# Kernel tuning notes

Hardware: AMD Instinct MI355X
Metric: run time of the kernel (lower is better)

Reference implementation:

```python
import jax, jax.numpy as jnp
import numpy as np

N = 5000          # ngenes / nodes
IN_DIM = 1280
H = 128           # hid_dim
E = 160000        # edges (before self-loops)
ALPHA = 0.2       # LeakyReLU slope (both module leakyrelu and GATv2 negative_slope)

def _glorot(key, shape):
    fan_in, fan_out = shape[0], shape[-1]
    lim = jnp.sqrt(6.0 / (fan_in + fan_out))
    return jax.random.uniform(key, shape, jnp.float32, -lim, lim)

def setup_inputs() -> dict:
    key = jax.random.key(0)
    ks = jax.random.split(key, 12)
    x = jax.random.normal(ks[0], (N, IN_DIM), jnp.float32)
    edge_index = jax.random.randint(ks[1], (2, E), 0, N, jnp.int64)
    return {
        "x": x,
        "edge_index": edge_index,
        "W_in": _glorot(ks[2], (IN_DIM, H)),
        "b_in": jnp.zeros((H,), jnp.float32),
        "W_l": _glorot(ks[3], (H, H)),
        "b_l": jnp.zeros((H,), jnp.float32),
        "W_r": _glorot(ks[4], (H, H)),
        "b_r": jnp.zeros((H,), jnp.float32),
        "att": _glorot(ks[5], (H, 1))[:, 0],
        "gat_bias": jnp.zeros((H,), jnp.float32),
        "W1": _glorot(ks[6], (N * H, H)),
        "b1": jnp.zeros((H,), jnp.float32),
        "W2": _glorot(ks[7], (H, 1)),
        "b2": jnp.zeros((1,), jnp.float32),
    }

def _leaky(v):
    return jnp.where(v >= 0, v, ALPHA * v)

def _gatv2(x, edge_index, W_l, b_l, W_r, b_r, att, gat_bias):
    # add self loops (PyG default)
    loop = jnp.arange(N, dtype=edge_index.dtype)
    src = jnp.concatenate([edge_index[0], loop])  # j: source of message
    dst = jnp.concatenate([edge_index[1], loop])  # i: target / softmax segment
    xl = x @ W_l + b_l                             # [N, H] (messages)
    xr = x @ W_r + b_r                             # [N, H] (target side)
    e = _leaky(xl[src] + xr[dst])                  # [E+N, H]
    score = e @ att                                # [E+N]
    # segment softmax over incoming edges of each dst node
    m = jax.ops.segment_max(score, dst, num_segments=N)
    ex = jnp.exp(score - m[dst])
    s = jax.ops.segment_sum(ex, dst, num_segments=N)
    a = ex / s[dst]                                # [E+N]
    out = jax.ops.segment_sum(a[:, None] * xl[src], dst, num_segments=N)
    return out + gat_bias

def reference(x, edge_index, W_in, b_in, W_l, b_l, W_r, b_r, att, gat_bias, W1, b1, W2, b2):
    h = jax.nn.relu(x @ W_in + b_in)                               # [N, H]
    h = _leaky(_gatv2(h, edge_index, W_l, b_l, W_r, b_r, att, gat_bias))
    h = h.reshape(-1)                                              # [N*H]
    h = jax.nn.relu(h @ W1 + b1)                                   # [H]
    return h @ W2 + b2                                             # [1]
```

## Files before the change

kernel.cpp:

```cpp
#include <hip/hip_runtime.h>
#include <math.h>

#define N_NODES 5000
#define IN_DIM  1280
#define HID     128
#define ALPHA   0.2f

typedef float f4v __attribute__((ext_vector_type(4)));

__device__ __forceinline__ float leaky(float v) { return v >= 0.f ? v : ALPHA * v; }

__global__ __launch_bounds__(256) void k_gemm_in(const float* __restrict__ x,
    const float* __restrict__ W, float* __restrict__ hp) {
  const int col  = threadIdx.x & 127;
  const int rg   = threadIdx.x >> 7;
  const int row0 = blockIdx.x * 8;
  const int kbase = blockIdx.y * 640;
  __shared__ float xs[8][128];
  float acc[4] = {0.f,0.f,0.f,0.f};
  for (int k0 = 0; k0 < 640; k0 += 128) {
#pragma unroll
    for (int t = 0; t < 4; ++t) {
      int idx = threadIdx.x + t * 256;
      int r = idx >> 7, cc = idx & 127;
      xs[r][cc] = x[(size_t)(row0 + r) * IN_DIM + kbase + k0 + cc];
    }
    __syncthreads();
#pragma unroll 8
    for (int kq = 0; kq < 32; ++kq) {
      const int kk = kbase + k0 + kq * 4;
      const float w0 = W[(kk + 0) * HID + col];
      const float w1 = W[(kk + 1) * HID + col];
      const float w2 = W[(kk + 2) * HID + col];
      const float w3 = W[(kk + 3) * HID + col];
#pragma unroll
      for (int r = 0; r < 4; ++r) {
        const f4v xv = *reinterpret_cast<const f4v*>(&xs[rg * 4 + r][kq * 4]);
        acc[r] = fmaf(xv.x, w0, acc[r]);
        acc[r] = fmaf(xv.y, w1, acc[r]);
        acc[r] = fmaf(xv.z, w2, acc[r]);
        acc[r] = fmaf(xv.w, w3, acc[r]);
      }
    }
    __syncthreads();
  }
  float* o = hp + (size_t)blockIdx.y * N_NODES * HID;
#pragma unroll
  for (int r = 0; r < 4; ++r)
    o[(size_t)(row0 + rg * 4 + r) * HID + col] = acc[r];
}

__global__ __launch_bounds__(256) void k_gemm_lr(const float* __restrict__ hp,
    const float* __restrict__ bin,
    const float* __restrict__ Wl, const float* __restrict__ bl,
    const float* __restrict__ Wr, const float* __restrict__ br,
    float* __restrict__ xl, float* __restrict__ xr) {
  const int col  = threadIdx.x & 127;
  const int rg   = threadIdx.x >> 7;
  const int row0 = blockIdx.x * 8;
  __shared__ float hs[8][128];
  const float* hp0 = hp;
  const float* hp1 = hp + (size_t)N_NODES * HID;
#pragma unroll
  for (int t = 0; t < 4; ++t) {
    int idx = threadIdx.x + t * 256;
    int r = idx >> 7, c = idx & 127;
    size_t g = (size_t)(row0 + r) * HID + c;
    hs[r][c] = fmaxf(hp0[g] + hp1[g] + bin[c], 0.f);
  }
  __syncthreads();
  float accl[4] = {0.f,0.f,0.f,0.f};
  float accr[4] = {0.f,0.f,0.f,0.f};
#pragma unroll 4
  for (int kq = 0; kq < 32; ++kq) {
    float wl0 = Wl[(kq*4+0)*HID + col], wr0 = Wr[(kq*4+0)*HID + col];
    float wl1 = Wl[(kq*4+1)*HID + col], wr1 = Wr[(kq*4+1)*HID + col];
    float wl2 = Wl[(kq*4+2)*HID + col], wr2 = Wr[(kq*4+2)*HID + col];
    float wl3 = Wl[(kq*4+3)*HID + col], wr3 = Wr[(kq*4+3)*HID + col];
#pragma unroll
    for (int r = 0; r < 4; ++r) {
      const f4v xv = *reinterpret_cast<const f4v*>(&hs[rg*4 + r][kq*4]);
      accl[r] = fmaf(xv.x, wl0, accl[r]); accr[r] = fmaf(xv.x, wr0, accr[r]);
      accl[r] = fmaf(xv.y, wl1, accl[r]); accr[r] = fmaf(xv.y, wr1, accr[r]);
      accl[r] = fmaf(xv.z, wl2, accl[r]); accr[r] = fmaf(xv.z, wr2, accr[r]);
      accl[r] = fmaf(xv.w, wl3, accl[r]); accr[r] = fmaf(xv.w, wr3, accr[r]);
    }
  }
  const float biasl = bl[col], biasr = br[col];
#pragma unroll
  for (int r = 0; r < 4; ++r) {
    int row = row0 + rg * 4 + r;
    xl[(size_t)row * HID + col] = accl[r] + biasl;
    xr[(size_t)row * HID + col] = accr[r] + biasr;
  }
}

__global__ __launch_bounds__(256) void k_hist(const int* __restrict__ ei, int E, int ET,
                                              unsigned* __restrict__ deg) {
  int e = blockIdx.x * blockDim.x + threadIdx.x;
  if (e >= ET) return;
  const int dst = (e < E) ? ei[E + e] : (e - E);
  atomicAdd(&deg[dst], 1u);
}

__global__ __launch_bounds__(256) void k_scan(const unsigned* __restrict__ deg,
    unsigned* __restrict__ off, unsigned* __restrict__ cursor) {
  __shared__ unsigned part[256];
  const int t = threadIdx.x;
  unsigned s = 0;
#pragma unroll
  for (int i = 0; i < 20; ++i) { int d = t * 20 + i; if (d < N_NODES) s += deg[d]; }
  part[t] = s;
  __syncthreads();
  for (int st = 1; st < 256; st <<= 1) {
    unsigned val = (t >= st) ? part[t - st] : 0u;
    __syncthreads();
    part[t] += val;
    __syncthreads();
  }
  unsigned run = (t == 0) ? 0u : part[t - 1];
  for (int i = 0; i < 20; ++i) {
    int d = t * 20 + i;
    if (d < N_NODES) { off[d] = run; cursor[d] = run; run += deg[d]; }
  }
}

__global__ __launch_bounds__(256) void k_fill(const int* __restrict__ ei, int E, int ET,
    unsigned* __restrict__ cursor, unsigned* __restrict__ csr) {
  int e = blockIdx.x * blockDim.x + threadIdx.x;
  if (e >= ET) return;
  const int src = (e < E) ? ei[e]     : (e - E);
  const int dst = (e < E) ? ei[E + e] : (e - E);
  unsigned pos = atomicAdd(&cursor[dst], 1u);
  csr[pos] = (unsigned)src;
}

__global__ __launch_bounds__(64) void k_agg(const float* __restrict__ xl,
    const float* __restrict__ xr, const float* __restrict__ att,
    const float* __restrict__ gb, const unsigned* __restrict__ off,
    const unsigned* __restrict__ deg, const unsigned* __restrict__ csr,
    float* __restrict__ v) {
  const int dst  = blockIdx.x;
  const int lane = threadIdx.x;
  const unsigned o  = off[dst];
  const unsigned dg = deg[dst];
  const float2 xr2 = *reinterpret_cast<const float2*>(&xr[(size_t)dst * HID + lane * 2]);
  const float2 at2 = *reinterpret_cast<const float2*>(&att[lane * 2]);
  float m = -INFINITY, s = 0.f;
  float2 acc = make_float2(0.f, 0.f);
  for (unsigned t = 0; t < dg; ++t) {
    const unsigned src = csr[o + t];
    const float2 xl2 = *reinterpret_cast<const float2*>(&xl[(size_t)src * HID + lane * 2]);
    float sa = leaky(xl2.x + xr2.x) * at2.x + leaky(xl2.y + xr2.y) * at2.y;
#pragma unroll
    for (int st = 1; st < 64; st <<= 1) sa += __shfl_xor(sa, st);
    if (sa > m) {
      const float sc = __expf(m - sa);
      s = s * sc + 1.f;
      acc.x = acc.x * sc + xl2.x;
      acc.y = acc.y * sc + xl2.y;
      m = sa;
    } else {
      const float ex = __expf(sa - m);
      s += ex;
      acc.x = fmaf(ex, xl2.x, acc.x);
      acc.y = fmaf(ex, xl2.y, acc.y);
    }
  }
  const float inv = 1.f / s;
  const float2 gb2 = *reinterpret_cast<const float2*>(&gb[lane * 2]);
  float2 r;
  r.x = leaky(fmaf(acc.x, inv, gb2.x));
  r.y = leaky(fmaf(acc.y, inv, gb2.y));
  *reinterpret_cast<float2*>(&v[(size_t)dst * HID + lane * 2]) = r;
}

__global__ __launch_bounds__(256) void k_matvec(const float* __restrict__ v,
    const float* __restrict__ W1, float* __restrict__ out128) {
  const int c  = threadIdx.x & 31;
  const int rr = threadIdx.x >> 5;
  const int base = blockIdx.x * 320;
  __shared__ float vs[320];
  if (threadIdx.x < 256) vs[threadIdx.x] = v[base + threadIdx.x];
  if (threadIdx.x < 64)  vs[256 + threadIdx.x] = v[base + 256 + threadIdx.x];
  __syncthreads();
  const float* Wp = W1 + (size_t)(base + rr) * HID + c * 4;
  f4v pf[8];
#pragma unroll
  for (int p = 0; p < 8; ++p)
    pf[p] = __builtin_nontemporal_load(reinterpret_cast<const f4v*>(Wp + (size_t)p * 8 * HID));
  f4v acc = {0.f, 0.f, 0.f, 0.f};
#pragma unroll
  for (int i = 0; i < 40; ++i) {
    const f4v w = pf[i & 7];
    if (i + 8 < 40)
      pf[i & 7] = __builtin_nontemporal_load(
          reinterpret_cast<const f4v*>(Wp + (size_t)(i + 8) * 8 * HID));
    const float vv = vs[i * 8 + rr];
    acc.x = fmaf(vv, w.x, acc.x);
    acc.y = fmaf(vv, w.y, acc.y);
    acc.z = fmaf(vv, w.z, acc.z);
    acc.w = fmaf(vv, w.w, acc.w);
  }
  __shared__ float part[8][128];
  *reinterpret_cast<f4v*>(&part[rr][c * 4]) = acc;
  __syncthreads();
  if (rr == 0) {
    f4v sum = {0.f, 0.f, 0.f, 0.f};
#pragma unroll
    for (int g = 0; g < 8; ++g) {
      const f4v p = *reinterpret_cast<const f4v*>(&part[g][c * 4]);
      sum.x += p.x; sum.y += p.y; sum.z += p.z; sum.w += p.w;
    }
    atomicAdd(&out128[c * 4 + 0], sum.x);
    atomicAdd(&out128[c * 4 + 1], sum.y);
    atomicAdd(&out128[c * 4 + 2], sum.z);
    atomicAdd(&out128[c * 4 + 3], sum.w);
  }
}

__global__ void k_final(const float* __restrict__ out128, const float* __restrict__ b1,
                        const float* __restrict__ W2, const float* __restrict__ b2,
                        float* __restrict__ out) {
  __shared__ float red[128];
  const int j = threadIdx.x;
  const float y = fmaxf(out128[j] + b1[j], 0.f);
  red[j] = y * W2[j];
  __syncthreads();
  if (j == 0) {
    float t = 0.f;
    for (int k = 0; k < 128; ++k) t += red[k];
    out[0] = t + b2[0];
  }
}

extern "C" void kernel_launch(void* const* d_in, const int* in_sizes, int n_in,
                              void* d_out, int out_size, void* d_ws, size_t ws_size,
                              hipStream_t stream) {
  const float* x    = (const float*)d_in[0];
  const int*   ei   = (const int*)  d_in[1];
  const float* W_in = (const float*)d_in[2];
  const float* b_in = (const float*)d_in[3];
  const float* W_l  = (const float*)d_in[4];
  const float* b_l  = (const float*)d_in[5];
  const float* W_r  = (const float*)d_in[6];
  const float* b_r  = (const float*)d_in[7];
  const float* att  = (const float*)d_in[8];
  const float* gb   = (const float*)d_in[9];
  const float* W1   = (const float*)d_in[10];
  const float* b1   = (const float*)d_in[11];
  const float* W2   = (const float*)d_in[12];
  const float* b2   = (const float*)d_in[13];
  float* out = (float*)d_out;

  const int E  = in_sizes[1] / 2;
  const int ET = E + N_NODES;

  float* ws = (float*)d_ws;
  float*    hp     = ws;
  float*    xl     = ws + 1280000;
  float*    xr     = ws + 1920000;
  float*    v      = ws + 2560000;
  unsigned* deg    = (unsigned*)(ws + 3200000);
  float*    out128 = ws + 3200000 + N_NODES;
  unsigned* off    = (unsigned*)(out128 + HID);
  unsigned* cursor = off + N_NODES;
  unsigned* csr    = cursor + N_NODES;

  hipMemsetAsync(deg, 0, (size_t)(N_NODES + HID) * sizeof(unsigned), stream);

  k_gemm_in <<<dim3(N_NODES / 8, 2), 256, 0, stream>>>(x, W_in, hp);
  k_gemm_lr <<<N_NODES / 8, 256, 0, stream>>>(hp, b_in, W_l, b_l, W_r, b_r, xl, xr);
  k_hist    <<<(ET + 255) / 256, 256, 0, stream>>>(ei, E, ET, deg);
  k_scan    <<<1, 256, 0, stream>>>(deg, off, cursor);
  k_fill    <<<(ET + 255) / 256, 256, 0, stream>>>(ei, E, ET, cursor, csr);
  k_agg     <<<N_NODES, 64, 0, stream>>>(xl, xr, att, gb, off, deg, csr, v);
  k_matvec  <<<2000, 256, 0, stream>>>(v, W1, out128);
  k_final   <<<1, 128, 0, stream>>>(out128, b1, W2, b2, out);
}
```

Before: 763.0 us.

## Restructure W1 matvec as grid-stride streaming with fixed 1024-block grid

The big matvec over W1 (about 327 MB) now uses a flat grid-stride pattern. Each thread streams float4 elements of W1 with 8 loads in flight per outer step and fetches the matching v entry per element, replacing the per-block row tiling with shared-memory v staging. Zeroing of out128 moves into the scan kernel, and the final reduction uses wave shuffles. The intent is better sustained HBM bandwidth with fewer, longer-lived blocks, at the cost of more scattered, redundant v reads.

```diff
diff --git a/kernel.cpp b/kernel.cpp
--- a/kernel.cpp
+++ b/kernel.cpp
@@ -5,6 +5,7 @@
 #define IN_DIM  1280
 #define HID     128
 #define ALPHA   0.2f
+#define NF4     20480000
 
 typedef float f4v __attribute__((ext_vector_type(4)));
 
@@ -104,9 +105,11 @@
 }
 
 __global__ __launch_bounds__(256) void k_scan(const unsigned* __restrict__ deg,
-    unsigned* __restrict__ off, unsigned* __restrict__ cursor) {
+    unsigned* __restrict__ off, unsigned* __restrict__ cursor,
+    float* __restrict__ out128) {
   __shared__ unsigned part[256];
   const int t = threadIdx.x;
+  if (t < HID) out128[t] = 0.f;
   unsigned s = 0;
 #pragma unroll
   for (int i = 0; i < 20; ++i) { int d = t * 20 + i; if (d < N_NODES) s += deg[d]; }
@@ -177,61 +180,58 @@
 
 __global__ __launch_bounds__(256) void k_matvec(const float* __restrict__ v,
     const float* __restrict__ W1, float* __restrict__ out128) {
-  const int c  = threadIdx.x & 31;
-  const int rr = threadIdx.x >> 5;
-  const int base = blockIdx.x * 320;
-  __shared__ float vs[320];
-  if (threadIdx.x < 256) vs[threadIdx.x] = v[base + threadIdx.x];
-  if (threadIdx.x < 64)  vs[256 + threadIdx.x] = v[base + 256 + threadIdx.x];
-  __syncthreads();
-  const float* Wp = W1 + (size_t)(base + rr) * HID + c * 4;
-  f4v pf[8];
-#pragma unroll
-  for (int p = 0; p < 8; ++p)
-    pf[p] = __builtin_nontemporal_load(reinterpret_cast<const f4v*>(Wp + (size_t)p * 8 * HID));
+  const int tid = blockIdx.x * 256 + threadIdx.x;
+  const int NT  = 1024 * 256;
+  const f4v* W4 = reinterpret_cast<const f4v*>(W1);
   f4v acc = {0.f, 0.f, 0.f, 0.f};
 #pragma unroll
-  for (int i = 0; i < 40; ++i) {
-    const f4v w = pf[i & 7];
-    if (i + 8 < 40)
-      pf[i & 7] = __builtin_nontemporal_load(
-          reinterpret_cast<const f4v*>(Wp + (size_t)(i + 8) * 8 * HID));
-    const float vv = vs[i * 8 + rr];
-    acc.x = fmaf(vv, w.x, acc.x);
-    acc.y = fmaf(vv, w.y, acc.y);
-    acc.z = fmaf(vv, w.z, acc.z);
-    acc.w = fmaf(vv, w.w, acc.w);
+  for (int o = 0; o < 10; ++o) {
+    f4v  w[8]; float vv[8]; int idx[8]; bool ok[8];
+#pragma unroll
+    for (int u = 0; u < 8; ++u) {
+      idx[u] = tid + (o * 8 + u) * NT;
+      ok[u]  = idx[u] < NF4;
+      if (ok[u]) w[u] = __builtin_nontemporal_load(&W4[idx[u]]);
+    }
+#pragma unroll
+    for (int u = 0; u < 8; ++u) if (ok[u]) vv[u] = v[idx[u] >> 5];
+#pragma unroll
+    for (int u = 0; u < 8; ++u) if (ok[u]) {
+      acc.x = fmaf(vv[u], w[u].x, acc.x);
+      acc.y = fmaf(vv[u], w[u].y, acc.y);
+      acc.z = fmaf(vv[u], w[u].z, acc.z);
+      acc.w = fmaf(vv[u], w[u].w, acc.w);
+    }
   }
   __shared__ float part[8][128];
-  *reinterpret_cast<f4v*>(&part[rr][c * 4]) = acc;
+  const int q = threadIdx.x & 31, rr = threadIdx.x >> 5;
+  *reinterpret_cast<f4v*>(&part[rr][q * 4]) = acc;
   __syncthreads();
   if (rr == 0) {
-    f4v sum = {0.f, 0.f, 0.f, 0.f};
+    f4v s = {0.f, 0.f, 0.f, 0.f};
 #pragma unroll
     for (int g = 0; g < 8; ++g) {
-      const f4v p = *reinterpret_cast<const f4v*>(&part[g][c * 4]);
-      sum.x += p.x; sum.y += p.y; sum.z += p.z; sum.w += p.w;
-    }
-    atomicAdd(&out128[c * 4 + 0], sum.x);
-    atomicAdd(&out128[c * 4 + 1], sum.y);
-    atomicAdd(&out128[c * 4 + 2], sum.z);
-    atomicAdd(&out128[c * 4 + 3], sum.w);
+      const f4v p = *reinterpret_cast<const f4v*>(&part[g][q * 4]);
+      s.x += p.x; s.y += p.y; s.z += p.z; s.w += p.w;
+    }
+    atomicAdd(&out128[q * 4 + 0], s.x);
+    atomicAdd(&out128[q * 4 + 1], s.y);
+    atomicAdd(&out128[q * 4 + 2], s.z);
+    atomicAdd(&out128[q * 4 + 3], s.w);
   }
 }
 
 __global__ void k_final(const float* __restrict__ out128, const float* __restrict__ b1,
                         const float* __restrict__ W2, const float* __restrict__ b2,
                         float* __restrict__ out) {
-  __shared__ float red[128];
   const int j = threadIdx.x;
-  const float y = fmaxf(out128[j] + b1[j], 0.f);
-  red[j] = y * W2[j];
-  __syncthreads();
-  if (j == 0) {
-    float t = 0.f;
-    for (int k = 0; k < 128; ++k) t += red[k];
-    out[0] = t + b2[0];
-  }
+  float y = fmaxf(out128[j] + b1[j], 0.f) * W2[j];
+  __shared__ float red[2];
+#pragma unroll
+  for (int st = 32; st > 0; st >>= 1) y += __shfl_down(y, st);
+  if ((j & 63) == 0) red[j >> 6] = y;
+  __syncthreads();
+  if (j == 0) out[0] = red[0] + red[1] + b2[0];
 }
 
 extern "C" void kernel_launch(void* const* d_in, const int* in_sizes, int n_in,
@@ -267,14 +267,14 @@
   unsigned* cursor = off + N_NODES;
   unsigned* csr    = cursor + N_NODES;
 
-  hipMemsetAsync(deg, 0, (size_t)(N_NODES + HID) * sizeof(unsigned), stream);
+  hipMemsetAsync(deg, 0, (size_t)N_NODES * sizeof(unsigned), stream);
 
   k_gemm_in <<<dim3(N_NODES / 8, 2), 256, 0, stream>>>(x, W_in, hp);
   k_gemm_lr <<<N_NODES / 8, 256, 0, stream>>>(hp, b_in, W_l, b_l, W_r, b_r, xl, xr);
   k_hist    <<<(ET + 255) / 256, 256, 0, stream>>>(ei, E, ET, deg);
-  k_scan    <<<1, 256, 0, stream>>>(deg, off, cursor);
+  k_scan    <<<1, 256, 0, stream>>>(deg, off, cursor, out128);
   k_fill    <<<(ET + 255) / 256, 256, 0, stream>>>(ei, E, ET, cursor, csr);
   k_agg     <<<N_NODES, 64, 0, stream>>>(xl, xr, att, gb, off, deg, csr, v);
-  k_matvec  <<<2000, 256, 0, stream>>>(v, W1, out128);
+  k_matvec  <<<1024, 256, 0, stream>>>(v, W1, out128);
   k_final   <<<1, 128, 0, stream>>>(out128, b1, W2, b2, out);
 }
```

After: 1.238 ms. 1.62x slower.
